# Optimization experiments

Measured on AMD Instinct MI355X. Metric: run time of the kernel, lower is better.

## Reference

```python
import jax, jax.numpy as jnp
import numpy as np

# dims
B, L, C = 2, 2048, 256          # batch, seq_len (== max_length), input_dim
H, D = 8, 32                     # num_head, head_dim
W = 3                            # avg-pool window along key axis


def setup_inputs() -> dict:
    key = jax.random.key(0)
    ks = jax.random.split(key, 7)
    g_qk = (2.0 / (C + H * D)) ** 0.5   # GlorotNormal std
    g_v = (2.0 / (C + H)) ** 0.5
    g_pe = (2.0 / (L + C)) ** 0.5
    return {
        "x":  jax.random.normal(ks[0], (B, L, C), dtype=jnp.float32),
        "Wq": jax.random.normal(ks[1], (C, H * D), dtype=jnp.float32) * g_qk,
        "bq": jnp.zeros((H, 1, 1, D), dtype=jnp.float32),
        "Wk": jax.random.normal(ks[2], (C, H * D), dtype=jnp.float32) * g_qk,
        "bk": jnp.zeros((H, 1, 1, D), dtype=jnp.float32),
        "Wv": jax.random.normal(ks[3], (C, H), dtype=jnp.float32) * g_v,
        "pe": jax.random.normal(ks[4], (L, C), dtype=jnp.float32) * g_pe,
    }


def reference(x, Wq, bq, Wk, bk, Wv, pe):
    b, l, _ = x.shape
    xq = x + pe                                   # (B,L,C) -- pe added to q and k inputs only
    q = (xq @ Wq).reshape(b, l, H, D).transpose(2, 0, 1, 3) + bq   # (H,B,L,D)
    k = (xq @ Wk).reshape(b, l, H, D).transpose(2, 0, 1, 3) + bk   # (H,B,L,D)
    v = (x @ Wv).transpose(2, 0, 1)               # (H,B,L) scalar gate per (head, pos)

    attn = jnp.einsum('hbqd,hbkd->hbqk', q, k) * (float(D) ** -0.5)  # (H,B,Lq,Lk)
    attn = jax.nn.softmax(attn, axis=-1)
    # band_part(-1, 0): keep lower triangle (q >= k), applied AFTER softmax
    causal = jnp.tril(jnp.ones((l, l), dtype=bool))
    attn = jnp.where(causal, attn, jnp.zeros((), attn.dtype))
    # scalar value gate along the query axis
    attn = attn * v[..., None]                    # (H,B,Lq,Lk)
    # avg-pool window W along key axis, SAME padding, pads excluded from count (TF semantics)
    sums = jax.lax.reduce_window(attn, 0.0, jax.lax.add, (1, 1, 1, W), (1, 1, 1, 1), 'SAME')
    counts = jax.lax.reduce_window(jnp.ones((l,), attn.dtype), 0.0, jax.lax.add, (W,), (1,), 'SAME')
    attn = sums / counts                          # broadcast (Lk,) over (H,B,Lq,Lk)
    # permute to (B,Lq,Lk,H) then global_mode sum over Lq  ->  (B,Lk,H)
    return jnp.sum(attn, axis=2).transpose(1, 2, 0)
```

## Files before the change

kernel.cpp:

```cpp
#include <hip/hip_runtime.h>

#define B 2
#define L 2048
#define C 256
#define H 8
#define D 32
#define HB 16
#define SCALE 0.17677669529663687f
#define LOG2E 1.4426950408889634f
#define QS (SCALE * LOG2E)

using bf16x8 = __attribute__((ext_vector_type(8))) __bf16;
using f32x4  = __attribute__((ext_vector_type(4))) float;

static __device__ inline unsigned short f2bf(float f) {
    unsigned u = __float_as_uint(f);
    return (unsigned short)((u + 0x7fffu + ((u >> 16) & 1u)) >> 16);
}
static __device__ inline unsigned pk2(float lo, float hi) {
    return (unsigned)f2bf(lo) | ((unsigned)f2bf(hi) << 16);
}

static __device__ inline float fexp2(float x) {
#if __has_builtin(__builtin_amdgcn_exp2f)
    return __builtin_amdgcn_exp2f(x);
#else
    float r; asm("v_exp_f32 %0, %1" : "=v"(r) : "v"(x)); return r;
#endif
}

__global__ __launch_bounds__(256) void prep_kernel(
    const float* __restrict__ x,
    const float* __restrict__ Wq,
    const float* __restrict__ Wk,
    const float* __restrict__ Wv,
    unsigned short* __restrict__ WqT,
    unsigned short* __restrict__ WkT,
    float* __restrict__ Vo)
{
    __shared__ float smem[256 * 8 + 4 * 8 * 8];
    const int t = threadIdx.x;

    if (blockIdx.x < 512) {
        float (*xrT)[8] = (float(*)[8])smem;
        float* vred = smem + 256 * 8;
        const int row0 = blockIdx.x * 8;
        const int b = row0 >> 11;
#pragma unroll
        for (int i = 0; i < 8; ++i)
            xrT[t][i] = x[(row0 + i) * C + t];
        __syncthreads();
        {
            const int cc = t >> 6, sub = t & 63, vi = sub >> 3, vh = sub & 7;
            float va = 0.f;
            for (int c = cc * 64; c < cc * 64 + 64; ++c)
                va += xrT[c][vi] * Wv[c * H + vh];
            vred[(cc * 8 + vi) * 8 + vh] = va;
        }
        __syncthreads();
        if (t < 64) {
            const int i2 = t >> 3, h2 = t & 7;
            const float v = vred[(0 * 8 + i2) * 8 + h2] + vred[(1 * 8 + i2) * 8 + h2] +
                            vred[(2 * 8 + i2) * 8 + h2] + vred[(3 * 8 + i2) * 8 + h2];
            const int l = (row0 + i2) & (L - 1);
            Vo[(h2 * B + b) * L + l] = v;
        }
    } else {
        const int bb = blockIdx.x - 512;
        const int mat = bb >> 5;
        const int fid = (bb & 31) * 256 + t;
        const int col = fid & 15;
        const int quad = (fid >> 4) & 3;
        const int kk = (fid >> 6) & 7;
        const int nt = fid >> 9;
        const int n = nt * 16 + col;
        const int c0 = kk * 32 + quad * 8;
        const float* W = mat ? Wk : Wq;
        unsigned short* WT = mat ? WkT : WqT;
        const float s = mat ? 1.0f : QS;

        float v[8];
#pragma unroll
        for (int j = 0; j < 8; ++j)
            v[j] = W[(c0 + j) * (H * D) + n] * s;
        uint4 u;
        u.x = pk2(v[0], v[1]); u.y = pk2(v[2], v[3]);
        u.z = pk2(v[4], v[5]); u.w = pk2(v[6], v[7]);
        *(uint4*)(WT + (size_t)fid * 8) = u;
    }
}

__global__ __launch_bounds__(256) void qk_gemm_kernel(
    const float* __restrict__ x, const float* __restrict__ pe,
    const unsigned short* __restrict__ WqT, const unsigned short* __restrict__ WkT,
    const float* __restrict__ bq, const float* __restrict__ bk,
    unsigned short* __restrict__ Qo, unsigned short* __restrict__ Ko)
{
    __shared__ uint4 xqs[16][32];
    const int t = threadIdx.x;
    const int w = t >> 6, lane = t & 63;
    const int quad = lane >> 4, col = lane & 15;
    const int row0 = (blockIdx.x >> 2) * 16;
    const int quarter = blockIdx.x & 3;

    {
        const int srow = t >> 4, sc = (t & 15) * 16;
        const int grow = row0 + srow;
        const int gl = grow & (L - 1);
        const float* xp = x + (size_t)grow * C + sc;
        const float* pp = pe + (size_t)gl * C + sc;
        const float4 a0 = ((const float4*)xp)[0], a1 = ((const float4*)xp)[1];
        const float4 a2 = ((const float4*)xp)[2], a3 = ((const float4*)xp)[3];
        const float4 p0 = ((const float4*)pp)[0], p1 = ((const float4*)pp)[1];
        const float4 p2 = ((const float4*)pp)[2], p3 = ((const float4*)pp)[3];
        uint4 u0, u1;
        u0.x = pk2(a0.x + p0.x, a0.y + p0.y);
        u0.y = pk2(a0.z + p0.z, a0.w + p0.w);
        u0.z = pk2(a1.x + p1.x, a1.y + p1.y);
        u0.w = pk2(a1.z + p1.z, a1.w + p1.w);
        u1.x = pk2(a2.x + p2.x, a2.y + p2.y);
        u1.y = pk2(a2.z + p2.z, a2.w + p2.w);
        u1.z = pk2(a3.x + p3.x, a3.y + p3.y);
        u1.w = pk2(a3.z + p3.z, a3.w + p3.w);
        const int cb = (t & 15) * 2;
        xqs[srow][(cb + 0) ^ (srow & 7)] = u0;
        xqs[srow][(cb + 1) ^ (srow & 7)] = u1;
    }
    __syncthreads();

    bf16x8 af[8];
#pragma unroll
    for (int kk = 0; kk < 8; ++kk)
        af[kk] = *(const bf16x8*)&xqs[col][(kk * 4 + quad) ^ (col & 7)];

    const int nt = quarter * 4 + w;
    const unsigned short* wq = WqT + (size_t)nt * 8 * 512;
    const unsigned short* wk = WkT + (size_t)nt * 8 * 512;
    const int foff = (quad * 16 + col) * 8;
    f32x4 accq = {0.f, 0.f, 0.f, 0.f};
    f32x4 acck = {0.f, 0.f, 0.f, 0.f};
#pragma unroll
    for (int kk = 0; kk < 8; ++kk) {
        const bf16x8 bq8 = *(const bf16x8*)(wq + kk * 512 + foff);
        const bf16x8 bk8 = *(const bf16x8*)(wk + kk * 512 + foff);
        accq = __builtin_amdgcn_mfma_f32_16x16x32_bf16(af[kk], bq8, accq, 0, 0, 0);
        acck = __builtin_amdgcn_mfma_f32_16x16x32_bf16(af[kk], bk8, acck, 0, 0, 0);
    }

    const int n = nt * 16 + col;
    const int h = n >> 5, d = n & 31;
    const float bqv = bq[n] * QS;
    const float bkv = bk[n];
#pragma unroll
    for (int r = 0; r < 4; ++r) {
        const int m = quad * 4 + r;
        const int grow = row0 + m, b = grow >> 11, l = grow & (L - 1);
        const size_t o = ((size_t)(h * B + b) * L + l) * D + d;
        Qo[o] = f2bf(accq[r] + bqv);
        Ko[o] = f2bf(acck[r] + bkv);
    }
}

__global__ __launch_bounds__(256) void passA_kernel(
    const __bf16* __restrict__ Qb, const __bf16* __restrict__ Kb,
    const float* __restrict__ V, float* __restrict__ G)
{
    __shared__ float lredA[4][4][4][16];
    __shared__ float lredB[4][4][4][16];
    const int tid = threadIdx.x;
    const int w = tid >> 6, lane = tid & 63;
    const int quad = lane >> 4, col = lane & 15;
    const int xcd = blockIdx.x & 7, g = blockIdx.x >> 3;
    const int hb = xcd * 2 + (g >> 6), p = g & 63;
    const __bf16* Qp = Qb + (size_t)hb * L * D;
    const __bf16* Kp = Kb + (size_t)hb * L * D;

    const bf16x8 qfa = *(const bf16x8*)(Qp + ((2 * p) * 16 + col) * D + quad * 8);
    const bf16x8 qfb = *(const bf16x8*)(Qp + ((2 * p + 1) * 16 + col) * D + quad * 8);
    const f32x4 zero = {0.f, 0.f, 0.f, 0.f};

    float la0 = 0.f, la1 = 0.f, la2 = 0.f, la3 = 0.f;
    float lb0 = 0.f, lb1 = 0.f, lb2 = 0.f, lb3 = 0.f;
    const __bf16* kp = Kp + (w * 512 + col) * D + quad * 8;
#pragma unroll 4
    for (int kt = 0; kt < 32; ++kt) {
        const bf16x8 kf = *(const bf16x8*)kp;
        kp += 16 * D;
        f32x4 a = __builtin_amdgcn_mfma_f32_16x16x32_bf16(qfa, kf, zero, 0, 0, 0);
        f32x4 bb = __builtin_amdgcn_mfma_f32_16x16x32_bf16(qfb, kf, zero, 0, 0, 0);
        la0 += fexp2(a[0]);  lb0 += fexp2(bb[0]);
        la1 += fexp2(a[1]);  lb1 += fexp2(bb[1]);
        la2 += fexp2(a[2]);  lb2 += fexp2(bb[2]);
        la3 += fexp2(a[3]);  lb3 += fexp2(bb[3]);
    }
    lredA[w][quad][0][col] = la0;  lredB[w][quad][0][col] = lb0;
    lredA[w][quad][1][col] = la1;  lredB[w][quad][1][col] = lb1;
    lredA[w][quad][2][col] = la2;  lredB[w][quad][2][col] = lb2;
    lredA[w][quad][3][col] = la3;  lredB[w][quad][3][col] = lb3;
    __syncthreads();
    if (tid < 32) {
        const int r8 = tid & 15;
        const int qd = r8 >> 2, r = r8 & 3;
        const float* base = (tid < 16) ? &lredA[0][0][0][0] : &lredB[0][0][0][0];
        float s = 0.f;
#pragma unroll
        for (int w2 = 0; w2 < 4; ++w2) {
            const float* pp = base + ((w2 * 4 + qd) * 4 + r) * 16;
#pragma unroll
            for (int c2 = 0; c2 < 16; ++c2) s += pp[c2];
        }
        const int qt = 2 * p + (tid >> 4);
        const int qq = hb * L + qt * 16 + r8;
        G[qq] = V[qq] / s;
    }
}

__global__ __launch_bounds__(256) void passB_kernel(
    const __bf16* __restrict__ Qb, const __bf16* __restrict__ Kb,
    const float* __restrict__ G, float* __restrict__ S)
{
    __shared__ float sred[2][4][4][16];
    const int tid = threadIdx.x;
    const int w = tid >> 6, lane = tid & 63;
    const int quad = lane >> 4, col = lane & 15;
    const int xcd = blockIdx.x & 7, g = blockIdx.x >> 3;
    const int hb = xcd * 2 + (g >> 6), p = g & 63;
    const int kb0 = 2 * p, kb1 = 2 * p + 1;
    const __bf16* Qp = Qb + (size_t)hb * L * D;
    const __bf16* Kp = Kb + (size_t)hb * L * D;
    const float* Gp = G + hb * L;

    const bf16x8 kf0 = *(const bf16x8*)(Kp + (kb0 * 16 + col) * D + quad * 8);
    const bf16x8 kf1 = *(const bf16x8*)(Kp + (kb1 * 16 + col) * D + quad * 8);
    const f32x4 zero = {0.f, 0.f, 0.f, 0.f};
    const int kidx0 = kb0 * 16 + col;
    const int kidx1 = kb1 * 16 + col;

    float s0 = 0.f, s1 = 0.f;
    int qt = kb0 + w;
    if (qt < 128) {
        const bf16x8 qf = *(const bf16x8*)(Qp + (qt * 16 + col) * D + quad * 8);
        const float4 gg = *(const float4*)(Gp + qt * 16 + quad * 4);
        const int qbase = qt * 16 + quad * 4;
        f32x4 a0 = __builtin_amdgcn_mfma_f32_16x16x32_bf16(qf, kf0, zero, 0, 0, 0);
        if (w == 0) {
            s0 += (qbase + 0 >= kidx0) ? fexp2(a0[0]) * gg.x : 0.f;
            s0 += (qbase + 1 >= kidx0) ? fexp2(a0[1]) * gg.y : 0.f;
            s0 += (qbase + 2 >= kidx0) ? fexp2(a0[2]) * gg.z : 0.f;
            s0 += (qbase + 3 >= kidx0) ? fexp2(a0[3]) * gg.w : 0.f;
        } else {
            s0 += fexp2(a0[0]) * gg.x + fexp2(a0[1]) * gg.y +
                  fexp2(a0[2]) * gg.z + fexp2(a0[3]) * gg.w;
            f32x4 a1 = __builtin_amdgcn_mfma_f32_16x16x32_bf16(qf, kf1, zero, 0, 0, 0);
            if (w == 1) {
                s1 += (qbase + 0 >= kidx1) ? fexp2(a1[0]) * gg.x : 0.f;
                s1 += (qbase + 1 >= kidx1) ? fexp2(a1[1]) * gg.y : 0.f;
                s1 += (qbase + 2 >= kidx1) ? fexp2(a1[2]) * gg.z : 0.f;
                s1 += (qbase + 3 >= kidx1) ? fexp2(a1[3]) * gg.w : 0.f;
            } else {
                s1 += fexp2(a1[0]) * gg.x + fexp2(a1[1]) * gg.y +
                      fexp2(a1[2]) * gg.z + fexp2(a1[3]) * gg.w;
            }
        }
        qt += 4;
    }
    for (; qt < 128; qt += 4) {
        const bf16x8 qf = *(const bf16x8*)(Qp + (qt * 16 + col) * D + quad * 8);
        const float4 gg = *(const float4*)(Gp + qt * 16 + quad * 4);
        f32x4 a0 = __builtin_amdgcn_mfma_f32_16x16x32_bf16(qf, kf0, zero, 0, 0, 0);
        f32x4 a1 = __builtin_amdgcn_mfma_f32_16x16x32_bf16(qf, kf1, zero, 0, 0, 0);
        s0 += fexp2(a0[0]) * gg.x + fexp2(a0[1]) * gg.y +
              fexp2(a0[2]) * gg.z + fexp2(a0[3]) * gg.w;
        s1 += fexp2(a1[0]) * gg.x + fexp2(a1[1]) * gg.y +
              fexp2(a1[2]) * gg.z + fexp2(a1[3]) * gg.w;
    }
    sred[0][w][quad][col] = s0;
    sred[1][w][quad][col] = s1;
    __syncthreads();
    if (tid < 32) {
        const int c = tid & 15, which = tid >> 4;
        float s = 0.f;
#pragma unroll
        for (int j = 0; j < 16; ++j) s += sred[which][j >> 2][j & 3][c];
        S[hb * L + (2 * p + which) * 16 + c] = s;
    }
}

__global__ __launch_bounds__(256) void pool_kernel(
    const float* __restrict__ S, float* __restrict__ out)
{
    const int flat = blockIdx.x * 256 + threadIdx.x;
    const int h = flat & 7;
    const int k = (flat >> 3) & (L - 1);
    const int b = flat >> 14;
    const float* Sb = S + (h * B + b) * L;
    float s = Sb[k];
    float cnt = 1.f;
    if (k > 0)     { s += Sb[k - 1]; cnt += 1.f; }
    if (k < L - 1) { s += Sb[k + 1]; cnt += 1.f; }
    out[flat] = s / cnt;
}

extern "C" void kernel_launch(void* const* d_in, const int* in_sizes, int n_in,
                              void* d_out, int out_size, void* d_ws, size_t ws_size,
                              hipStream_t stream)
{
    const float* x  = (const float*)d_in[0];
    const float* Wq = (const float*)d_in[1];
    const float* bq = (const float*)d_in[2];
    const float* Wk = (const float*)d_in[3];
    const float* bk = (const float*)d_in[4];
    const float* Wv = (const float*)d_in[5];
    const float* pe = (const float*)d_in[6];
    float* out = (float*)d_out;

    unsigned short* Qbf = (unsigned short*)d_ws;
    unsigned short* Kbf = Qbf + (size_t)HB * L * D;
    float* Vo = (float*)(Kbf + (size_t)HB * L * D);
    float* G  = Vo + (size_t)HB * L;
    float* S  = G  + (size_t)HB * L;
    unsigned short* WqT = (unsigned short*)(S + (size_t)HB * L);
    unsigned short* WkT = WqT + (size_t)C * H * D;

    prep_kernel<<<576, 256, 0, stream>>>(x, Wq, Wk, Wv, WqT, WkT, Vo);
    qk_gemm_kernel<<<1024, 256, 0, stream>>>(x, pe, WqT, WkT, bq, bk, Qbf, Kbf);
    passA_kernel<<<1024, 256, 0, stream>>>(
        (const __bf16*)Qbf, (const __bf16*)Kbf, Vo, G);
    passB_kernel<<<1024, 256, 0, stream>>>(
        (const __bf16*)Qbf, (const __bf16*)Kbf, G, S);
    pool_kernel<<<(B * L * H) / 256, 256, 0, stream>>>(S, out);
}
```

Before: 102.4 us.

## Fuse V projection into passA and pooling into passB via last-block counter

Moves the x@Wv gate computation out of the prep kernel into passA, where each block computes its own 32 rows of V for its head, and shrinks prep to a small weight-transpose kernel. The pool kernel is removed: each passB block bumps a per-(head,batch) atomic counter, and the last block to finish does the 3-wide average pool for that row. This removes one launch and shortens the prep kernel, at the cost of redundant x reads in passA (each head recomputes its V slice) and a serialized tail where a single block per head-batch does the pooling.

```diff
diff --git a/kernel.cpp b/kernel.cpp
--- a/kernel.cpp
+++ b/kernel.cpp
@@ -29,65 +29,36 @@
 #endif
 }
 
-__global__ __launch_bounds__(256) void prep_kernel(
-    const float* __restrict__ x,
+__global__ __launch_bounds__(256) void wtrans_kernel(
     const float* __restrict__ Wq,
     const float* __restrict__ Wk,
-    const float* __restrict__ Wv,
     unsigned short* __restrict__ WqT,
     unsigned short* __restrict__ WkT,
-    float* __restrict__ Vo)
-{
-    __shared__ float smem[256 * 8 + 4 * 8 * 8];
+    unsigned int* __restrict__ cnt)
+{
     const int t = threadIdx.x;
-
-    if (blockIdx.x < 512) {
-        float (*xrT)[8] = (float(*)[8])smem;
-        float* vred = smem + 256 * 8;
-        const int row0 = blockIdx.x * 8;
-        const int b = row0 >> 11;
-#pragma unroll
-        for (int i = 0; i < 8; ++i)
-            xrT[t][i] = x[(row0 + i) * C + t];
-        __syncthreads();
-        {
-            const int cc = t >> 6, sub = t & 63, vi = sub >> 3, vh = sub & 7;
-            float va = 0.f;
-            for (int c = cc * 64; c < cc * 64 + 64; ++c)
-                va += xrT[c][vi] * Wv[c * H + vh];
-            vred[(cc * 8 + vi) * 8 + vh] = va;
-        }
-        __syncthreads();
-        if (t < 64) {
-            const int i2 = t >> 3, h2 = t & 7;
-            const float v = vred[(0 * 8 + i2) * 8 + h2] + vred[(1 * 8 + i2) * 8 + h2] +
-                            vred[(2 * 8 + i2) * 8 + h2] + vred[(3 * 8 + i2) * 8 + h2];
-            const int l = (row0 + i2) & (L - 1);
-            Vo[(h2 * B + b) * L + l] = v;
-        }
-    } else {
-        const int bb = blockIdx.x - 512;
-        const int mat = bb >> 5;
-        const int fid = (bb & 31) * 256 + t;
-        const int col = fid & 15;
-        const int quad = (fid >> 4) & 3;
-        const int kk = (fid >> 6) & 7;
-        const int nt = fid >> 9;
-        const int n = nt * 16 + col;
-        const int c0 = kk * 32 + quad * 8;
-        const float* W = mat ? Wk : Wq;
-        unsigned short* WT = mat ? WkT : WqT;
-        const float s = mat ? 1.0f : QS;
-
-        float v[8];
-#pragma unroll
-        for (int j = 0; j < 8; ++j)
-            v[j] = W[(c0 + j) * (H * D) + n] * s;
-        uint4 u;
-        u.x = pk2(v[0], v[1]); u.y = pk2(v[2], v[3]);
-        u.z = pk2(v[4], v[5]); u.w = pk2(v[6], v[7]);
-        *(uint4*)(WT + (size_t)fid * 8) = u;
-    }
+    if (blockIdx.x == 0 && t < HB) cnt[t] = 0;
+
+    const int mat = blockIdx.x >> 5;
+    const int fid = (blockIdx.x & 31) * 256 + t;
+    const int col = fid & 15;
+    const int quad = (fid >> 4) & 3;
+    const int kk = (fid >> 6) & 7;
+    const int nt = fid >> 9;
+    const int n = nt * 16 + col;
+    const int c0 = kk * 32 + quad * 8;
+    const float* W = mat ? Wk : Wq;
+    unsigned short* WT = mat ? WkT : WqT;
+    const float s = mat ? 1.0f : QS;
+
+    float v[8];
+#pragma unroll
+    for (int j = 0; j < 8; ++j)
+        v[j] = W[(c0 + j) * (H * D) + n] * s;
+    uint4 u;
+    u.x = pk2(v[0], v[1]); u.y = pk2(v[2], v[3]);
+    u.z = pk2(v[4], v[5]); u.w = pk2(v[6], v[7]);
+    *(uint4*)(WT + (size_t)fid * 8) = u;
 }
 
 __global__ __launch_bounds__(256) void qk_gemm_kernel(
@@ -163,10 +134,12 @@
 
 __global__ __launch_bounds__(256) void passA_kernel(
     const __bf16* __restrict__ Qb, const __bf16* __restrict__ Kb,
-    const float* __restrict__ V, float* __restrict__ G)
+    const float* __restrict__ x, const float* __restrict__ Wv,
+    float* __restrict__ G)
 {
     __shared__ float lredA[4][4][4][16];
     __shared__ float lredB[4][4][4][16];
+    __shared__ float vpart[32][8];
     const int tid = threadIdx.x;
     const int w = tid >> 6, lane = tid & 63;
     const int quad = lane >> 4, col = lane & 15;
@@ -193,6 +166,20 @@
         la2 += fexp2(a[2]);  lb2 += fexp2(bb[2]);
         la3 += fexp2(a[3]);  lb3 += fexp2(bb[3]);
     }
+
+    {
+        const int i = tid >> 3, j = tid & 7;
+        const int hh = hb >> 1, bb2 = hb & 1;
+        const float* xp = x + ((size_t)(bb2 * L + 32 * p + i)) * C;
+        float va = 0.f;
+#pragma unroll 8
+        for (int m = 0; m < 32; ++m) {
+            const int c = j + 8 * m;
+            va += xp[c] * Wv[c * H + hh];
+        }
+        vpart[i][j] = va;
+    }
+
     lredA[w][quad][0][col] = la0;  lredB[w][quad][0][col] = lb0;
     lredA[w][quad][1][col] = la1;  lredB[w][quad][1][col] = lb1;
     lredA[w][quad][2][col] = la2;  lredB[w][quad][2][col] = lb2;
@@ -209,17 +196,22 @@
 #pragma unroll
             for (int c2 = 0; c2 < 16; ++c2) s += pp[c2];
         }
+        const float v = vpart[tid][0] + vpart[tid][1] + vpart[tid][2] +
+                        vpart[tid][3] + vpart[tid][4] + vpart[tid][5] +
+                        vpart[tid][6] + vpart[tid][7];
         const int qt = 2 * p + (tid >> 4);
         const int qq = hb * L + qt * 16 + r8;
-        G[qq] = V[qq] / s;
+        G[qq] = v / s;
     }
 }
 
 __global__ __launch_bounds__(256) void passB_kernel(
     const __bf16* __restrict__ Qb, const __bf16* __restrict__ Kb,
-    const float* __restrict__ G, float* __restrict__ S)
+    const float* __restrict__ G, float* __restrict__ S,
+    unsigned int* __restrict__ cnt, float* __restrict__ out)
 {
     __shared__ float sred[2][4][4][16];
+    __shared__ int lastf;
     const int tid = threadIdx.x;
     const int w = tid >> 6, lane = tid & 63;
     const int quad = lane >> 4, col = lane & 15;
@@ -284,21 +276,27 @@
         for (int j = 0; j < 16; ++j) s += sred[which][j >> 2][j & 3][c];
         S[hb * L + (2 * p + which) * 16 + c] = s;
     }
-}
-
-__global__ __launch_bounds__(256) void pool_kernel(
-    const float* __restrict__ S, float* __restrict__ out)
-{
-    const int flat = blockIdx.x * 256 + threadIdx.x;
-    const int h = flat & 7;
-    const int k = (flat >> 3) & (L - 1);
-    const int b = flat >> 14;
-    const float* Sb = S + (h * B + b) * L;
-    float s = Sb[k];
-    float cnt = 1.f;
-    if (k > 0)     { s += Sb[k - 1]; cnt += 1.f; }
-    if (k < L - 1) { s += Sb[k + 1]; cnt += 1.f; }
-    out[flat] = s / cnt;
+    __syncthreads();
+    if (tid == 0) {
+        __threadfence();
+        const unsigned old = atomicAdd(&cnt[hb], 1u);
+        lastf = (old == 63u);
+    }
+    __syncthreads();
+    if (lastf) {
+        __threadfence();
+        const int h = hb >> 1, b = hb & 1;
+        const float* Sb = S + (size_t)hb * L;
+#pragma unroll
+        for (int i = 0; i < 8; ++i) {
+            const int k = i * 256 + tid;
+            float s = Sb[k];
+            float n = 1.f;
+            if (k > 0)     { s += Sb[k - 1]; n += 1.f; }
+            if (k < L - 1) { s += Sb[k + 1]; n += 1.f; }
+            out[((size_t)b * L + k) * H + h] = s / n;
+        }
+    }
 }
 
 extern "C" void kernel_launch(void* const* d_in, const int* in_sizes, int n_in,
@@ -316,17 +314,16 @@
 
     unsigned short* Qbf = (unsigned short*)d_ws;
     unsigned short* Kbf = Qbf + (size_t)HB * L * D;
-    float* Vo = (float*)(Kbf + (size_t)HB * L * D);
-    float* G  = Vo + (size_t)HB * L;
-    float* S  = G  + (size_t)HB * L;
+    float* G  = (float*)(Kbf + (size_t)HB * L * D);
+    float* S  = G + (size_t)HB * L;
     unsigned short* WqT = (unsigned short*)(S + (size_t)HB * L);
     unsigned short* WkT = WqT + (size_t)C * H * D;
-
-    prep_kernel<<<576, 256, 0, stream>>>(x, Wq, Wk, Wv, WqT, WkT, Vo);
+    unsigned int* cnt = (unsigned int*)(WkT + (size_t)C * H * D);
+
+    wtrans_kernel<<<64, 256, 0, stream>>>(Wq, Wk, WqT, WkT, cnt);
     qk_gemm_kernel<<<1024, 256, 0, stream>>>(x, pe, WqT, WkT, bq, bk, Qbf, Kbf);
     passA_kernel<<<1024, 256, 0, stream>>>(
-        (const __bf16*)Qbf, (const __bf16*)Kbf, Vo, G);
+        (const __bf16*)Qbf, (const __bf16*)Kbf, x, Wv, G);
     passB_kernel<<<1024, 256, 0, stream>>>(
-        (const __bf16*)Qbf, (const __bf16*)Kbf, G, S);
-    pool_kernel<<<(B * L * H) / 256, 256, 0, stream>>>(S, out);
-}
+        (const __bf16*)Qbf, (const __bf16*)Kbf, G, S, cnt, out);
+}
```

After: 124.2 us. +21.3%, slower.

## Fuse avg-pool into passB by recomputing halo key columns per block

Applied to the files above, without the earlier changes.

Removes the separate pool kernel and the S workspace. Each passB block now recomputes the attention column sums for the two halo keys next to its 32-key tile, using scalar dot products over all later queries. It then applies the 3-wide average in shared memory and writes the output directly. Block-to-tile mapping is also changed to pair light and heavy causal tiles for load balance. The cost is extra scalar, uncoalesced per-thread work on the halo columns in every block.

```diff
diff --git a/kernel.cpp b/kernel.cpp
--- a/kernel.cpp
+++ b/kernel.cpp
@@ -217,14 +217,18 @@
 
 __global__ __launch_bounds__(256) void passB_kernel(
     const __bf16* __restrict__ Qb, const __bf16* __restrict__ Kb,
-    const float* __restrict__ G, float* __restrict__ S)
+    const float* __restrict__ G, float* __restrict__ out)
 {
     __shared__ float sred[2][4][4][16];
+    __shared__ float bred[2][4];
+    __shared__ float spool[34];
     const int tid = threadIdx.x;
     const int w = tid >> 6, lane = tid & 63;
     const int quad = lane >> 4, col = lane & 15;
     const int xcd = blockIdx.x & 7, g = blockIdx.x >> 3;
-    const int hb = xcd * 2 + (g >> 6), p = g & 63;
+    const int hb = xcd * 2 + (g >> 6);
+    const int praw = g & 63;
+    const int p = (praw < 32) ? praw : 95 - praw;
     const int kb0 = 2 * p, kb1 = 2 * p + 1;
     const __bf16* Qp = Qb + (size_t)hb * L * D;
     const __bf16* Kp = Kb + (size_t)hb * L * D;
@@ -276,29 +280,61 @@
     }
     sred[0][w][quad][col] = s0;
     sred[1][w][quad][col] = s1;
+
+    const int k0 = 32 * p;
+    float bl = 0.f, br = 0.f;
+    if (p > 0) {
+        const int kL = k0 - 1;
+        const __bf16* kr = Kp + (size_t)kL * D;
+        for (int q = kL + tid; q < L; q += 256) {
+            const __bf16* qr = Qp + (size_t)q * D;
+            float s = 0.f;
+#pragma unroll
+            for (int d = 0; d < D; ++d) s += (float)qr[d] * (float)kr[d];
+            bl += fexp2(s) * Gp[q];
+        }
+    }
+    if (p < 63) {
+        const int kR = k0 + 32;
+        const __bf16* kr = Kp + (size_t)kR * D;
+        for (int q = kR + tid; q < L; q += 256) {
+            const __bf16* qr = Qp + (size_t)q * D;
+            float s = 0.f;
+#pragma unroll
+            for (int d = 0; d < D; ++d) s += (float)qr[d] * (float)kr[d];
+            br += fexp2(s) * Gp[q];
+        }
+    }
+#pragma unroll
+    for (int off = 1; off < 64; off <<= 1) {
+        bl += __shfl_xor(bl, off);
+        br += __shfl_xor(br, off);
+    }
+    if (lane == 0) { bred[0][w] = bl; bred[1][w] = br; }
     __syncthreads();
+
     if (tid < 32) {
         const int c = tid & 15, which = tid >> 4;
         float s = 0.f;
 #pragma unroll
         for (int j = 0; j < 16; ++j) s += sred[which][j >> 2][j & 3][c];
-        S[hb * L + (2 * p + which) * 16 + c] = s;
-    }
-}
-
-__global__ __launch_bounds__(256) void pool_kernel(
-    const float* __restrict__ S, float* __restrict__ out)
-{
-    const int flat = blockIdx.x * 256 + threadIdx.x;
-    const int h = flat & 7;
-    const int k = (flat >> 3) & (L - 1);
-    const int b = flat >> 14;
-    const float* Sb = S + (h * B + b) * L;
-    float s = Sb[k];
-    float cnt = 1.f;
-    if (k > 0)     { s += Sb[k - 1]; cnt += 1.f; }
-    if (k < L - 1) { s += Sb[k + 1]; cnt += 1.f; }
-    out[flat] = s / cnt;
+        spool[1 + tid] = s;
+    } else if (tid == 32) {
+        spool[0] = bred[0][0] + bred[0][1] + bred[0][2] + bred[0][3];
+    } else if (tid == 33) {
+        spool[33] = bred[1][0] + bred[1][1] + bred[1][2] + bred[1][3];
+    }
+    __syncthreads();
+
+    if (tid < 32) {
+        const int k = k0 + tid;
+        const int h2 = hb >> 1, b2 = hb & 1;
+        float s = spool[1 + tid];
+        float n = 1.f;
+        if (k > 0)     { s += spool[tid];     n += 1.f; }
+        if (k < L - 1) { s += spool[2 + tid]; n += 1.f; }
+        out[((size_t)b2 * L + k) * H + h2] = s / n;
+    }
 }
 
 extern "C" void kernel_launch(void* const* d_in, const int* in_sizes, int n_in,
@@ -318,8 +354,7 @@
     unsigned short* Kbf = Qbf + (size_t)HB * L * D;
     float* Vo = (float*)(Kbf + (size_t)HB * L * D);
     float* G  = Vo + (size_t)HB * L;
-    float* S  = G  + (size_t)HB * L;
-    unsigned short* WqT = (unsigned short*)(S + (size_t)HB * L);
+    unsigned short* WqT = (unsigned short*)(G + (size_t)HB * L);
     unsigned short* WkT = WqT + (size_t)C * H * D;
 
     prep_kernel<<<576, 256, 0, stream>>>(x, Wq, Wk, Wv, WqT, WkT, Vo);
@@ -327,6 +362,5 @@
     passA_kernel<<<1024, 256, 0, stream>>>(
         (const __bf16*)Qbf, (const __bf16*)Kbf, Vo, G);
     passB_kernel<<<1024, 256, 0, stream>>>(
-        (const __bf16*)Qbf, (const __bf16*)Kbf, G, S);
-    pool_kernel<<<(B * L * H) / 256, 256, 0, stream>>>(S, out);
-}
+        (const __bf16*)Qbf, (const __bf16*)Kbf, G, out);
+}
```

Measured after the change: 112.6 us. 1.1x slower.
